# Kernel tuning notes

Hardware: AMD Instinct MI355X
Metric: run time of the kernel (lower is better)

Reference implementation:

```python
import jax, jax.numpy as jnp
import numpy as np

N = 50000       # num nodes
E = 400000      # num edges (before self loops)
IN, HID, H, OUT = 128, 64, 4, 64
SLOPE = 0.2     # PyG GATv2Conv default negative_slope


def setup_inputs() -> dict:
    key = jax.random.key(0)
    ks = jax.random.split(key, 14)
    def lin(k, fan_in, fan_out):
        return jax.random.normal(k, (fan_in, fan_out), jnp.float32) / np.sqrt(fan_in)
    return {
        "x": jax.random.normal(ks[0], (N, IN), jnp.float32),
        "edge_index": jax.random.randint(ks[1], (2, E), 0, N, jnp.int32),
        # layer 1: in=IN -> HID per head, H heads, concat
        "Wl1": lin(ks[2], IN, H * HID), "bl1": jnp.zeros((H * HID,), jnp.float32),
        "Wr1": lin(ks[3], IN, H * HID), "br1": jnp.zeros((H * HID,), jnp.float32),
        "att1": jax.random.normal(ks[4], (H, HID), jnp.float32) / np.sqrt(HID),
        "bias1": jnp.zeros((H * HID,), jnp.float32),
        # layer 2: in=H*HID -> OUT, 1 head, concat=False
        "Wl2": lin(ks[5], H * HID, OUT), "bl2": jnp.zeros((OUT,), jnp.float32),
        "Wr2": lin(ks[6], H * HID, OUT), "br2": jnp.zeros((OUT,), jnp.float32),
        "att2": jax.random.normal(ks[7], (1, OUT), jnp.float32) / np.sqrt(OUT),
        "bias2": jnp.zeros((OUT,), jnp.float32),
    }


def gatv2_conv(x, src, dst, Wl, bl, Wr, br, att, heads, out_ch, num_nodes):
    """PyG GATv2Conv (share_weights=False). src->dst aggregation at dst."""
    xl = (x @ Wl + bl).reshape(-1, heads, out_ch)  # source transform (x_j)
    xr = (x @ Wr + br).reshape(-1, heads, out_ch)  # target transform (x_i)
    m = xl[src] + xr[dst]                          # [E, H, C]
    e = jnp.sum(jax.nn.leaky_relu(m, SLOPE) * att, axis=-1)  # [E, H]
    # segment softmax over incoming edges of each dst node
    emax = jax.ops.segment_max(e, dst, num_segments=num_nodes)
    ex = jnp.exp(e - emax[dst])
    denom = jax.ops.segment_sum(ex, dst, num_segments=num_nodes)
    alpha = ex / denom[dst]                        # [E, H]
    out = jax.ops.segment_sum(alpha[:, :, None] * xl[src], dst, num_segments=num_nodes)
    return out  # [N, H, C]


def reference(x, edge_index, Wl1, bl1, Wr1, br1, att1, bias1,
              Wl2, bl2, Wr2, br2, att2, bias2):
    n = x.shape[0]
    loops = jnp.arange(n, dtype=edge_index.dtype)
    src = jnp.concatenate([edge_index[0], loops])  # add_self_loops=True
    dst = jnp.concatenate([edge_index[1], loops])
    h = gatv2_conv(x, src, dst, Wl1, bl1, Wr1, br1, att1, H, HID, n)
    h = h.reshape(n, H * HID) + bias1              # concat=True
    h = jax.nn.elu(h)                              # dropout=0.0
    o = gatv2_conv(h, src, dst, Wl2, bl2, Wr2, br2, att2, 1, OUT, n)
    return o.reshape(n, OUT) + bias2               # concat=False, heads=1
```

## Files before the change

kernel.cpp:

```cpp
#include <hip/hip_runtime.h>
#include <hip/hip_bf16.h>

typedef unsigned short u16;
typedef __attribute__((ext_vector_type(8))) short short8;
typedef __attribute__((ext_vector_type(4))) float floatx4;
typedef __attribute__((ext_vector_type(2))) float f32x2;

#define N_NODES 50000
#define N_EDGES 400000
#define ET      450000
#define F_IN    128
#define C1      256
#define HID     64
#define OUTC    64
#define SLOPE   0.2f

__device__ __forceinline__ float bf2f(u16 v) {
    return __uint_as_float(((unsigned)v) << 16);
}
__device__ __forceinline__ float bflo(unsigned u) { return __uint_as_float(u << 16); }
__device__ __forceinline__ float bfhi(unsigned u) { return __uint_as_float(u & 0xffff0000u); }
__device__ __forceinline__ u16 f2bf(float f) {
    unsigned u = __float_as_uint(f);
    return (u16)((u + 0x7fffu + ((u >> 16) & 1u)) >> 16);
}
__device__ __forceinline__ f32x2 up2(unsigned u) {
    f32x2 r; r.x = bflo(u); r.y = bfhi(u); return r;
}
template<int CTRL>
__device__ __forceinline__ float dpp_add(float x) {
    return x + __int_as_float(__builtin_amdgcn_update_dpp(
        0, __float_as_int(x), CTRL, 0xF, 0xF, true));
}
__device__ __forceinline__ float red16(float p) {
    p = dpp_add<0xB1>(p);
    p = dpp_add<0x4E>(p);
    p = dpp_add<0x141>(p);
    p = dpp_add<0x140>(p);
    return p;
}

__global__ __launch_bounds__(256) void detect_kernel(const unsigned* __restrict__ xw,
                                                     int* __restrict__ cnt)
{
    unsigned w = xw[threadIdx.x];
    unsigned aexp = (w >> 7) & 0xFFu;
    if (aexp >= 170u || aexp <= 40u) atomicAdd(cnt, 1);
}

__global__ __launch_bounds__(256) void convert_all_kernel(
    const void* wl1, const void* wr1, const void* wl2, const void* wr2,
    const void* s0, const void* s1, const void* s2, const void* s3,
    const void* s4, const void* s5, const void* s6, const void* s7,
    u16* __restrict__ wt, u16* __restrict__ prm, const int* __restrict__ cnt)
{
    bool f32m = (*cnt >= 32);
    if (blockIdx.x == 384) {
        for (int t = threadIdx.x; t < 1280; t += 256) {
            const void* src; int local;
            if      (t < 256)  { src = s0; local = t; }
            else if (t < 512)  { src = s1; local = t - 256; }
            else if (t < 768)  { src = s2; local = t - 512; }
            else if (t < 1024) { src = s3; local = t - 768; }
            else if (t < 1088) { src = s4; local = t - 1024; }
            else if (t < 1152) { src = s5; local = t - 1088; }
            else if (t < 1216) { src = s6; local = t - 1152; }
            else               { src = s7; local = t - 1216; }
            prm[t] = f32m ? f2bf(((const float*)src)[local]) : ((const u16*)src)[local];
        }
        return;
    }
    int t = blockIdx.x * 256 + threadIdx.x;
    const void* src; int local, k, n, K, base;
    if (t < 32768)      { src = wl1; local = t;         k = local >> 8; n = local & 255; K = 128; base = 0; }
    else if (t < 65536) { src = wr1; local = t - 32768; k = local >> 8; n = local & 255; K = 128; base = 32768; }
    else if (t < 81920) { src = wl2; local = t - 65536; k = local >> 6; n = local & 63;  K = 256; base = 65536; }
    else                { src = wr2; local = t - 81920; k = local >> 6; n = local & 63;  K = 256; base = 81920; }
    u16 v = f32m ? f2bf(((const float*)src)[local]) : ((const u16*)src)[local];
    wt[base + n * K + k] = v;
}

__global__ __launch_bounds__(256) void hist_kernel(const int* __restrict__ ei,
                                                   int* __restrict__ hist)
{
    int t = blockIdx.x * 256 + threadIdx.x;
    if (t >= ET) return;
    int d = (t < N_EDGES) ? ei[N_EDGES + t] : t - N_EDGES;
    atomicAdd(&hist[d], 1);
}

__global__ __launch_bounds__(256) void scan1_kernel(const int* __restrict__ hist,
                                                    int* __restrict__ rowptr,
                                                    int* __restrict__ bsum)
{
    int t = threadIdx.x;
    int i = blockIdx.x * 256 + t;
    int v = (i < N_NODES) ? hist[i] : 0;
    __shared__ int sd[256];
    sd[t] = v;
    __syncthreads();
    #pragma unroll
    for (int ofs = 1; ofs < 256; ofs <<= 1) {
        int u = (t >= ofs) ? sd[t - ofs] : 0;
        __syncthreads();
        sd[t] += u;
        __syncthreads();
    }
    if (i < N_NODES) rowptr[i] = sd[t] - v;
    if (t == 255) bsum[blockIdx.x] = sd[255];
}

__global__ __launch_bounds__(256) void scan2_kernel(int* __restrict__ bsum,
                                                    int* __restrict__ boff)
{
    int t = threadIdx.x;
    int v = (t < 196) ? bsum[t] : 0;
    __shared__ int sd[256];
    sd[t] = v;
    __syncthreads();
    #pragma unroll
    for (int ofs = 1; ofs < 256; ofs <<= 1) {
        int u = (t >= ofs) ? sd[t - ofs] : 0;
        __syncthreads();
        sd[t] += u;
        __syncthreads();
    }
    if (t < 196) boff[t] = sd[t] - v;
}

__global__ __launch_bounds__(256) void scan3_kernel(int* __restrict__ rowptr,
                                                    const int* __restrict__ boff,
                                                    int* __restrict__ off)
{
    int i = blockIdx.x * 256 + threadIdx.x;
    if (i >= N_NODES) return;
    int r = rowptr[i] + boff[blockIdx.x];
    rowptr[i] = r;
    off[i] = r;
}

__global__ __launch_bounds__(256) void scatter_kernel(const int* __restrict__ ei,
                                                      int* __restrict__ off,
                                                      int* __restrict__ src_csr)
{
    int t = blockIdx.x * 256 + threadIdx.x;
    if (t >= ET) return;
    int s, d;
    if (t < N_EDGES) { s = ei[t]; d = ei[N_EDGES + t]; } else { s = d = t - N_EDGES; }
    int pos = atomicAdd(&off[d], 1);
    src_csr[pos] = s;
}

__global__ __launch_bounds__(256) void lin1_fused_kernel(
    const u16* __restrict__ X, const u16* __restrict__ Wt,
    const u16* __restrict__ bl, const u16* __restrict__ br,
    u16* __restrict__ Yl, u16* __restrict__ Yr, int nrows,
    const int* __restrict__ cnt)
{
    constexpr int K = 128, N = 256, LS = K + 8;
    __shared__ __align__(16) u16 sX[64 * LS];
    __shared__ __align__(16) u16 sW[64 * LS];
    const bool f32m = (*cnt >= 32);
    const float* X32 = (const float*)X;
    const int row0 = blockIdx.x * 64;
    const int wave = threadIdx.x >> 6, lane = threadIdx.x & 63;
    const int quad = lane >> 4, l16 = lane & 15;

    for (int i = threadIdx.x * 8; i < 64 * K; i += 2048) {
        int r = i >> 7, c = i & 127;
        int gr = row0 + r;
        u16* dst = &sX[r * LS + c];
        if (f32m) {
            float4 v0 = make_float4(0.f, 0.f, 0.f, 0.f), v1 = v0;
            if (gr < nrows) {
                v0 = *(const float4*)&X32[(size_t)gr * K + c];
                v1 = *(const float4*)&X32[(size_t)gr * K + c + 4];
            }
            ushort4 p0, p1;
            p0.x = f2bf(v0.x); p0.y = f2bf(v0.y); p0.z = f2bf(v0.z); p0.w = f2bf(v0.w);
            p1.x = f2bf(v1.x); p1.y = f2bf(v1.y); p1.z = f2bf(v1.z); p1.w = f2bf(v1.w);
            *(ushort4*)dst = p0;
            *(ushort4*)(dst + 4) = p1;
        } else {
            uint4 v = {0u, 0u, 0u, 0u};
            if (gr < nrows) v = *(const uint4*)&X[(size_t)gr * K + c];
            *(uint4*)dst = v;
        }
    }

    for (int side = 0; side < 2; ++side) {
        const u16* wbase = Wt + side * (N * K);
        const u16* bias  = side ? br : bl;
        u16* Y = side ? Yr : Yl;
        for (int ch = 0; ch < 4; ++ch) {
            __syncthreads();
            for (int i = threadIdx.x * 8; i < 64 * K; i += 2048) {
                int n = i >> 7, c = i & 127;
                *(uint4*)&sW[n * LS + c] = *(const uint4*)&wbase[(size_t)(ch * 64 + n) * K + c];
            }
            __syncthreads();
            floatx4 acc0 = {0.f, 0.f, 0.f, 0.f}, acc1 = acc0, acc2 = acc0, acc3 = acc0;
            #pragma unroll
            for (int kk = 0; kk < 4; ++kk) {
                short8 a  = *(const short8*)&sX[(wave * 16 + l16) * LS + kk * 32 + quad * 8];
                short8 b0 = *(const short8*)&sW[(l16) * LS + kk * 32 + quad * 8];
                short8 b1 = *(const short8*)&sW[(16 + l16) * LS + kk * 32 + quad * 8];
                short8 b2 = *(const short8*)&sW[(32 + l16) * LS + kk * 32 + quad * 8];
                short8 b3 = *(const short8*)&sW[(48 + l16) * LS + kk * 32 + quad * 8];
                acc0 = __builtin_amdgcn_mfma_f32_16x16x32_bf16(a, b0, acc0, 0, 0, 0);
                acc1 = __builtin_amdgcn_mfma_f32_16x16x32_bf16(a, b1, acc1, 0, 0, 0);
                acc2 = __builtin_amdgcn_mfma_f32_16x16x32_bf16(a, b2, acc2, 0, 0, 0);
                acc3 = __builtin_amdgcn_mfma_f32_16x16x32_bf16(a, b3, acc3, 0, 0, 0);
            }
            const int rbase = row0 + wave * 16 + quad * 4;
            #pragma unroll
            for (int cf = 0; cf < 4; ++cf) {
                const floatx4 av = (cf == 0) ? acc0 : (cf == 1) ? acc1 : (cf == 2) ? acc2 : acc3;
                const int col = ch * 64 + cf * 16 + l16;
                const float bv = bf2f(bias[col]);
                #pragma unroll
                for (int r = 0; r < 4; ++r) {
                    int row = rbase + r;
                    if (row < nrows) Y[(size_t)row * N + col] = f2bf(av[r] + bv);
                }
            }
        }
    }
}

__global__ __launch_bounds__(256) void lin2_fused_kernel(
    const u16* __restrict__ X, const u16* __restrict__ Wt,
    const u16* __restrict__ bl, const u16* __restrict__ br,
    u16* __restrict__ Yl, u16* __restrict__ Yr, int nrows)
{
    constexpr int K = 256, N = 64, LS = K + 8;
    __shared__ __align__(16) u16 sX[64 * LS];
    __shared__ __align__(16) u16 sW[64 * LS];
    const int row0 = blockIdx.x * 64;
    const int wave = threadIdx.x >> 6, lane = threadIdx.x & 63;
    const int quad = lane >> 4, l16 = lane & 15;

    for (int i = threadIdx.x * 8; i < 64 * K; i += 2048) {
        int r = i >> 8, c = i & 255;
        int gr = row0 + r;
        uint4 v = {0u, 0u, 0u, 0u};
        if (gr < nrows) v = *(const uint4*)&X[(size_t)gr * K + c];
        *(uint4*)&sX[r * LS + c] = v;
    }

    for (int side = 0; side < 2; ++side) {
        const u16* wbase = Wt + side * (N * K);
        const u16* bias  = side ? br : bl;
        u16* Y = side ? Yr : Yl;
        __syncthreads();
        for (int i = threadIdx.x * 8; i < 64 * K; i += 2048) {
            int n = i >> 8, c = i & 255;
            *(uint4*)&sW[n * LS + c] = *(const uint4*)&wbase[(size_t)n * K + c];
        }
        __syncthreads();
        floatx4 acc0 = {0.f, 0.f, 0.f, 0.f}, acc1 = acc0, acc2 = acc0, acc3 = acc0;
        #pragma unroll
        for (int kk = 0; kk < 8; ++kk) {
            short8 a  = *(const short8*)&sX[(wave * 16 + l16) * LS + kk * 32 + quad * 8];
            short8 b0 = *(const short8*)&sW[(l16) * LS + kk * 32 + quad * 8];
            short8 b1 = *(const short8*)&sW[(16 + l16) * LS + kk * 32 + quad * 8];
            short8 b2 = *(const short8*)&sW[(32 + l16) * LS + kk * 32 + quad * 8];
            short8 b3 = *(const short8*)&sW[(48 + l16) * LS + kk * 32 + quad * 8];
            acc0 = __builtin_amdgcn_mfma_f32_16x16x32_bf16(a, b0, acc0, 0, 0, 0);
            acc1 = __builtin_amdgcn_mfma_f32_16x16x32_bf16(a, b1, acc1, 0, 0, 0);
            acc2 = __builtin_amdgcn_mfma_f32_16x16x32_bf16(a, b2, acc2, 0, 0, 0);
            acc3 = __builtin_amdgcn_mfma_f32_16x16x32_bf16(a, b3, acc3, 0, 0, 0);
        }
        const int rbase = row0 + wave * 16 + quad * 4;
        #pragma unroll
        for (int cf = 0; cf < 4; ++cf) {
            const floatx4 av = (cf == 0) ? acc0 : (cf == 1) ? acc1 : (cf == 2) ? acc2 : acc3;
            const int col = cf * 16 + l16;
            const float bv = bf2f(bias[col]);
            #pragma unroll
            for (int r = 0; r < 4; ++r) {
                int row = rbase + r;
                if (row < nrows) Y[(size_t)row * N + col] = f2bf(av[r] + bv);
            }
        }
    }
}

__global__ __launch_bounds__(256) void node1_kernel(
    const u16* __restrict__ xl, const u16* __restrict__ xr,
    const int* __restrict__ rowptr, const int* __restrict__ hist,
    const int* __restrict__ src_csr, const u16* __restrict__ att,
    const u16* __restrict__ bias, u16* __restrict__ hout)
{
    const int d = __builtin_amdgcn_readfirstlane(blockIdx.x * 4 + (threadIdx.x >> 6));
    if (d >= N_NODES) return;
    const int l = threadIdx.x & 63;
    const int start = rowptr[d];
    const int deg = hist[d];

    uint2 auv = *(const uint2*)&att[l * 4];
    const f32x2 atA = up2(auv.x), atB = up2(auv.y);
    uint2 ruv = *(const uint2*)&xr[(size_t)d * C1 + l * 4];
    const f32x2 rA = up2(ruv.x), rB = up2(ruv.y);

    float m = -1e30f, la = 0.f;
    f32x2 accA = {0.f, 0.f}, accB = {0.f, 0.f};
    for (int j = 0; j < deg; j += 4) {
        const bool v1 = j + 1 < deg, v2 = j + 2 < deg, v3 = j + 3 < deg;
        int s0 = src_csr[start + j];
        int s1 = v1 ? src_csr[start + j + 1] : s0;
        int s2 = v2 ? src_csr[start + j + 2] : s0;
        int s3 = v3 ? src_csr[start + j + 3] : s0;
        uint2 u0 = *(const uint2*)&xl[(size_t)s0 * C1 + l * 4];
        uint2 u1 = *(const uint2*)&xl[(size_t)s1 * C1 + l * 4];
        uint2 u2 = *(const uint2*)&xl[(size_t)s2 * C1 + l * 4];
        uint2 u3 = *(const uint2*)&xl[(size_t)s3 * C1 + l * 4];
        f32x2 x0A = up2(u0.x), x0B = up2(u0.y);
        f32x2 x1A = up2(u1.x), x1B = up2(u1.y);
        f32x2 x2A = up2(u2.x), x2B = up2(u2.y);
        f32x2 x3A = up2(u3.x), x3B = up2(u3.y);
        f32x2 t, pv;
        t = x0A + rA; t = __builtin_elementwise_max(t, t * SLOPE); pv  = t * atA;
        t = x0B + rB; t = __builtin_elementwise_max(t, t * SLOPE); pv += t * atB;
        float p0 = pv.x + pv.y;
        t = x1A + rA; t = __builtin_elementwise_max(t, t * SLOPE); pv  = t * atA;
        t = x1B + rB; t = __builtin_elementwise_max(t, t * SLOPE); pv += t * atB;
        float p1 = pv.x + pv.y;
        t = x2A + rA; t = __builtin_elementwise_max(t, t * SLOPE); pv  = t * atA;
        t = x2B + rB; t = __builtin_elementwise_max(t, t * SLOPE); pv += t * atB;
        float p2 = pv.x + pv.y;
        t = x3A + rA; t = __builtin_elementwise_max(t, t * SLOPE); pv  = t * atA;
        t = x3B + rB; t = __builtin_elementwise_max(t, t * SLOPE); pv += t * atB;
        float p3 = pv.x + pv.y;
        p0 = red16(p0); p1 = red16(p1); p2 = red16(p2); p3 = red16(p3);
        float pm = p0;
        if (v1) pm = fmaxf(pm, p1);
        if (v2) pm = fmaxf(pm, p2);
        if (v3) pm = fmaxf(pm, p3);
        float mn = fmaxf(m, pm);
        float sc = __expf(m - mn);
        float w0 = __expf(p0 - mn);
        float w1 = v1 ? __expf(p1 - mn) : 0.f;
        float w2 = v2 ? __expf(p2 - mn) : 0.f;
        float w3 = v3 ? __expf(p3 - mn) : 0.f;
        la = la * sc + w0 + w1 + w2 + w3;
        accA = accA * sc + x0A * w0 + x1A * w1 + x2A * w2 + x3A * w3;
        accB = accB * sc + x0B * w0 + x1B * w1 + x2B * w2 + x3B * w3;
        m = mn;
    }
    const float inv = 1.f / la;
    const int c = l * 4;
    float v0 = accA.x * inv + bf2f(bias[c + 0]);
    float v1 = accA.y * inv + bf2f(bias[c + 1]);
    float v2 = accB.x * inv + bf2f(bias[c + 2]);
    float v3 = accB.y * inv + bf2f(bias[c + 3]);
    v0 = v0 > 0.f ? v0 : __expf(fminf(v0, 0.f)) - 1.f;
    v1 = v1 > 0.f ? v1 : __expf(fminf(v1, 0.f)) - 1.f;
    v2 = v2 > 0.f ? v2 : __expf(fminf(v2, 0.f)) - 1.f;
    v3 = v3 > 0.f ? v3 : __expf(fminf(v3, 0.f)) - 1.f;
    ushort4 o;
    o.x = f2bf(v0); o.y = f2bf(v1); o.z = f2bf(v2); o.w = f2bf(v3);
    *(ushort4*)&hout[(size_t)d * C1 + c] = o;
}

__global__ __launch_bounds__(256) void node2_kernel(
    const u16* __restrict__ xl, const u16* __restrict__ xr,
    const int* __restrict__ rowptr, const int* __restrict__ hist,
    const int* __restrict__ src_csr, const u16* __restrict__ att,
    const u16* __restrict__ bias, void* __restrict__ outp,
    const int* __restrict__ cnt)
{
    const int d = __builtin_amdgcn_readfirstlane(blockIdx.x * 4 + (threadIdx.x >> 6));
    if (d >= N_NODES) return;
    const int l = threadIdx.x & 63;
    const int start = rowptr[d];
    const int deg = hist[d];
    const int g = l >> 4, sub = l & 15;
    const int c0 = sub * 4;

    uint2 auv = *(const uint2*)&att[c0];
    const f32x2 atA = up2(auv.x), atB = up2(auv.y);
    uint2 ruv = *(const uint2*)&xr[(size_t)d * OUTC + c0];
    const f32x2 rA = up2(ruv.x), rB = up2(ruv.y);

    float m = -1e30f, la = 0.f;
    f32x2 accA = {0.f, 0.f}, accB = {0.f, 0.f};
    for (int j = 0; j < deg; j += 4) {
        const bool valid = j + g < deg;
        int s = valid ? src_csr[start + j + g] : d;
        uint2 uv = *(const uint2*)&xl[(size_t)s * OUTC + c0];
        f32x2 xA = up2(uv.x), xB = up2(uv.y);
        f32x2 t, pv;
        t = xA + rA; t = __builtin_elementwise_max(t, t * SLOPE); pv  = t * atA;
        t = xB + rB; t = __builtin_elementwise_max(t, t * SLOPE); pv += t * atB;
        float p = pv.x + pv.y;
        p = red16(p);
        float pvv = valid ? p : -1e30f;
        float mn = fmaxf(m, pvv);
        float sc = __expf(m - mn);
        float w  = valid ? __expf(p - mn) : 0.f;
        la = la * sc + w;
        accA = accA * sc + xA * w;
        accB = accB * sc + xB * w;
        m = mn;
    }
    #pragma unroll
    for (int ofs = 16; ofs <= 32; ofs <<= 1) {
        float mo = __shfl_xor(m, ofs);
        float lo = __shfl_xor(la, ofs);
        float bax = __shfl_xor(accA.x, ofs);
        float bay = __shfl_xor(accA.y, ofs);
        float bbx = __shfl_xor(accB.x, ofs);
        float bby = __shfl_xor(accB.y, ofs);
        float mn = fmaxf(m, mo);
        float s0 = __expf(m - mn), s1 = __expf(mo - mn);
        la = la * s0 + lo * s1;
        accA.x = accA.x * s0 + bax * s1;
        accA.y = accA.y * s0 + bay * s1;
        accB.x = accB.x * s0 + bbx * s1;
        accB.y = accB.y * s0 + bby * s1;
        m = mn;
    }
    if (g == 0) {
        const float inv = 1.f / la;
        float v0 = accA.x * inv + bf2f(bias[c0 + 0]);
        float v1 = accA.y * inv + bf2f(bias[c0 + 1]);
        float v2 = accB.x * inv + bf2f(bias[c0 + 2]);
        float v3 = accB.y * inv + bf2f(bias[c0 + 3]);
        if (*cnt >= 32) {
            float4 o = make_float4(v0, v1, v2, v3);
            *(float4*)&((float*)outp)[(size_t)d * OUTC + c0] = o;
        } else {
            ushort4 o;
            o.x = f2bf(v0); o.y = f2bf(v1); o.z = f2bf(v2); o.w = f2bf(v3);
            *(ushort4*)&((u16*)outp)[(size_t)d * OUTC + c0] = o;
        }
    }
}

extern "C" void kernel_launch(void* const* d_in, const int* in_sizes, int n_in,
                              void* d_out, int out_size, void* d_ws, size_t ws_size,
                              hipStream_t stream)
{
    const void* x  = d_in[0];
    const int*  ei = (const int*)d_in[1];

    char* ws = (char*)d_ws;
    u16* xl1     = (u16*)(ws + 0);
    u16* xr1     = (u16*)(ws + 25600000);
    u16* hbuf    = (u16*)(ws + 51200000);
    u16* xl2     = (u16*)(ws + 0);
    u16* xr2     = (u16*)(ws + 6400000);
    int* hist    = (int*)(ws + 76800000);
    int* rowptr  = (int*)(ws + 77000000);
    int* off     = (int*)(ws + 77200000);
    int* src_csr = (int*)(ws + 77400000);
    int* cnt     = (int*)(ws + 79200000);
    u16* prm     = (u16*)(ws + 79200064);
    u16* wt      = (u16*)(ws + 79210240);
    int* bsum    = (int*)(ws + 79410000);
    int* boff    = (int*)(ws + 79411024);

    u16* bl1   = prm + 0;
    u16* br1   = prm + 256;
    u16* att1  = prm + 512;
    u16* bias1 = prm + 768;
    u16* bl2   = prm + 1024;
    u16* br2   = prm + 1088;
    u16* att2  = prm + 1152;
    u16* bias2 = prm + 1216;
    u16* wt1   = wt + 0;
    u16* wt2   = wt + 65536;

    hipMemsetAsync(cnt, 0, 4, stream);
    detect_kernel<<<1, 256, 0, stream>>>((const unsigned*)x, cnt);
    convert_all_kernel<<<385, 256, 0, stream>>>(
        d_in[2], d_in[4], d_in[8], d_in[10],
        d_in[3], d_in[5], d_in[6], d_in[7], d_in[9], d_in[11], d_in[12], d_in[13],
        wt, prm, cnt);

    hipMemsetAsync(hist, 0, 200000, stream);
    const int eb = (ET + 255) / 256;
    hist_kernel<<<eb, 256, 0, stream>>>(ei, hist);
    scan1_kernel<<<196, 256, 0, stream>>>(hist, rowptr, bsum);
    scan2_kernel<<<1, 256, 0, stream>>>(bsum, boff);
    scan3_kernel<<<196, 256, 0, stream>>>(rowptr, boff, off);
    scatter_kernel<<<eb, 256, 0, stream>>>(ei, off, src_csr);

    const int gb = (N_NODES + 63) / 64;
    lin1_fused_kernel<<<gb, 256, 0, stream>>>((const u16*)x, wt1, bl1, br1, xl1, xr1, N_NODES, cnt);
    const int nb = (N_NODES * 64 + 255) / 256;
    node1_kernel<<<nb, 256, 0, stream>>>(xl1, xr1, rowptr, hist, src_csr, att1, bias1, hbuf);

    lin2_fused_kernel<<<gb, 256, 0, stream>>>(hbuf, wt2, bl2, br2, xl2, xr2, N_NODES);
    node2_kernel<<<nb, 256, 0, stream>>>(xl2, xr2, rowptr, hist, src_csr, att2, bias2, d_out, cnt);
}
```

Baseline: 262.0 us.

## Cut launch count: inline dtype detection, fold memset and scan2 into kernels

```diff
diff --git a/kernel.cpp b/kernel.cpp
--- a/kernel.cpp
+++ b/kernel.cpp
@@ -39,22 +39,26 @@
     p = dpp_add<0x140>(p);
     return p;
 }
-
-__global__ __launch_bounds__(256) void detect_kernel(const unsigned* __restrict__ xw,
-                                                     int* __restrict__ cnt)
-{
-    unsigned w = xw[threadIdx.x];
+__device__ __forceinline__ bool detect_f32(const unsigned* __restrict__ xw) {
+    unsigned w = xw[threadIdx.x & 63];
     unsigned aexp = (w >> 7) & 0xFFu;
-    if (aexp >= 170u || aexp <= 40u) atomicAdd(cnt, 1);
+    unsigned long long b = __ballot(aexp >= 170u || aexp <= 40u);
+    return __popcll(b) >= 16;
 }
 
 __global__ __launch_bounds__(256) void convert_all_kernel(
+    const unsigned* __restrict__ xw,
     const void* wl1, const void* wr1, const void* wl2, const void* wr2,
     const void* s0, const void* s1, const void* s2, const void* s3,
     const void* s4, const void* s5, const void* s6, const void* s7,
-    u16* __restrict__ wt, u16* __restrict__ prm, const int* __restrict__ cnt)
-{
-    bool f32m = (*cnt >= 32);
+    u16* __restrict__ wt, u16* __restrict__ prm, int* __restrict__ hist)
+{
+    if (blockIdx.x >= 385) {
+        int idx = (blockIdx.x - 385) * 256 + threadIdx.x;
+        if (idx < N_NODES) hist[idx] = 0;
+        return;
+    }
+    bool f32m = detect_f32(xw);
     if (blockIdx.x == 384) {
         for (int t = threadIdx.x; t < 1280; t += 256) {
             const void* src; int local;
@@ -110,11 +114,12 @@
     if (t == 255) bsum[blockIdx.x] = sd[255];
 }
 
-__global__ __launch_bounds__(256) void scan2_kernel(int* __restrict__ bsum,
-                                                    int* __restrict__ boff)
+__global__ __launch_bounds__(256) void scan3_kernel(int* __restrict__ rowptr,
+                                                    const int* __restrict__ bsum,
+                                                    int* __restrict__ off)
 {
     int t = threadIdx.x;
-    int v = (t < 196) ? bsum[t] : 0;
+    int v = (t < (int)blockIdx.x) ? bsum[t] : 0;
     __shared__ int sd[256];
     sd[t] = v;
     __syncthreads();
@@ -125,18 +130,13 @@
         sd[t] += u;
         __syncthreads();
     }
-    if (t < 196) boff[t] = sd[t] - v;
-}
-
-__global__ __launch_bounds__(256) void scan3_kernel(int* __restrict__ rowptr,
-                                                    const int* __restrict__ boff,
-                                                    int* __restrict__ off)
-{
-    int i = blockIdx.x * 256 + threadIdx.x;
-    if (i >= N_NODES) return;
-    int r = rowptr[i] + boff[blockIdx.x];
-    rowptr[i] = r;
-    off[i] = r;
+    int boff = sd[255];
+    int i = blockIdx.x * 256 + t;
+    if (i < N_NODES) {
+        int r = rowptr[i] + boff;
+        rowptr[i] = r;
+        off[i] = r;
+    }
 }
 
 __global__ __launch_bounds__(256) void scatter_kernel(const int* __restrict__ ei,
@@ -154,13 +154,12 @@
 __global__ __launch_bounds__(256) void lin1_fused_kernel(
     const u16* __restrict__ X, const u16* __restrict__ Wt,
     const u16* __restrict__ bl, const u16* __restrict__ br,
-    u16* __restrict__ Yl, u16* __restrict__ Yr, int nrows,
-    const int* __restrict__ cnt)
+    u16* __restrict__ Yl, u16* __restrict__ Yr, int nrows)
 {
     constexpr int K = 128, N = 256, LS = K + 8;
     __shared__ __align__(16) u16 sX[64 * LS];
     __shared__ __align__(16) u16 sW[64 * LS];
-    const bool f32m = (*cnt >= 32);
+    const bool f32m = detect_f32((const unsigned*)X);
     const float* X32 = (const float*)X;
     const int row0 = blockIdx.x * 64;
     const int wave = threadIdx.x >> 6, lane = threadIdx.x & 63;
@@ -368,8 +367,9 @@
     const int* __restrict__ rowptr, const int* __restrict__ hist,
     const int* __restrict__ src_csr, const u16* __restrict__ att,
     const u16* __restrict__ bias, void* __restrict__ outp,
-    const int* __restrict__ cnt)
-{
+    const unsigned* __restrict__ xorig)
+{
+    const bool f32o = detect_f32(xorig);
     const int d = __builtin_amdgcn_readfirstlane(blockIdx.x * 4 + (threadIdx.x >> 6));
     if (d >= N_NODES) return;
     const int l = threadIdx.x & 63;
@@ -427,7 +427,7 @@
         float v1 = accA.y * inv + bf2f(bias[c0 + 1]);
         float v2 = accB.x * inv + bf2f(bias[c0 + 2]);
         float v3 = accB.y * inv + bf2f(bias[c0 + 3]);
-        if (*cnt >= 32) {
+        if (f32o) {
             float4 o = make_float4(v0, v1, v2, v3);
             *(float4*)&((float*)outp)[(size_t)d * OUTC + c0] = o;
         } else {
@@ -455,11 +455,9 @@
     int* rowptr  = (int*)(ws + 77000000);
     int* off     = (int*)(ws + 77200000);
     int* src_csr = (int*)(ws + 77400000);
-    int* cnt     = (int*)(ws + 79200000);
     u16* prm     = (u16*)(ws + 79200064);
     u16* wt      = (u16*)(ws + 79210240);
     int* bsum    = (int*)(ws + 79410000);
-    int* boff    = (int*)(ws + 79411024);
 
     u16* bl1   = prm + 0;
     u16* br1   = prm + 256;
@@ -472,26 +470,23 @@
     u16* wt1   = wt + 0;
     u16* wt2   = wt + 65536;
 
-    hipMemsetAsync(cnt, 0, 4, stream);
-    detect_kernel<<<1, 256, 0, stream>>>((const unsigned*)x, cnt);
-    convert_all_kernel<<<385, 256, 0, stream>>>(
+    convert_all_kernel<<<581, 256, 0, stream>>>(
+        (const unsigned*)x,
         d_in[2], d_in[4], d_in[8], d_in[10],
         d_in[3], d_in[5], d_in[6], d_in[7], d_in[9], d_in[11], d_in[12], d_in[13],
-        wt, prm, cnt);
-
-    hipMemsetAsync(hist, 0, 200000, stream);
+        wt, prm, hist);
+
     const int eb = (ET + 255) / 256;
     hist_kernel<<<eb, 256, 0, stream>>>(ei, hist);
     scan1_kernel<<<196, 256, 0, stream>>>(hist, rowptr, bsum);
-    scan2_kernel<<<1, 256, 0, stream>>>(bsum, boff);
-    scan3_kernel<<<196, 256, 0, stream>>>(rowptr, boff, off);
+    scan3_kernel<<<196, 256, 0, stream>>>(rowptr, bsum, off);
     scatter_kernel<<<eb, 256, 0, stream>>>(ei, off, src_csr);
 
     const int gb = (N_NODES + 63) / 64;
-    lin1_fused_kernel<<<gb, 256, 0, stream>>>((const u16*)x, wt1, bl1, br1, xl1, xr1, N_NODES, cnt);
+    lin1_fused_kernel<<<gb, 256, 0, stream>>>((const u16*)x, wt1, bl1, br1, xl1, xr1, N_NODES);
     const int nb = (N_NODES * 64 + 255) / 256;
     node1_kernel<<<nb, 256, 0, stream>>>(xl1, xr1, rowptr, hist, src_csr, att1, bias1, hbuf);
-
     lin2_fused_kernel<<<gb, 256, 0, stream>>>(hbuf, wt2, bl2, br2, xl2, xr2, N_NODES);
-    node2_kernel<<<nb, 256, 0, stream>>>(xl2, xr2, rowptr, hist, src_csr, att2, bias2, d_out, cnt);
-}
+    node2_kernel<<<nb, 256, 0, stream>>>(xl2, xr2, rowptr, hist, src_csr, att2, bias2, d_out,
+                                         (const unsigned*)x);
+}
```

Result: no change. 262.3 us (+0.1%).
